# Performance work log

Measured on AMD Instinct MI355X. Metric: run time of the kernel, lower is better.

The kernel has to match this reference:

```python
import jax, jax.numpy as jnp
import numpy as np

N_NODES = 10000
N_EDGES = 100000
C = 64          # in_channels == out_channels (required by x_i + x_m)
D_EDGE = 16     # edge_attr feature dim


def setup_inputs() -> dict:
    key = jax.random.key(0)
    k_x, k_ei, k_ea, k_w, k_b, k_r, k_bias = jax.random.split(key, 7)
    x = jax.random.normal(k_x, (N_NODES, C), dtype=jnp.float32)
    edge_index = jax.random.randint(k_ei, (2, N_EDGES), 0, N_NODES, dtype=jnp.int32)
    edge_attr = jax.random.normal(k_ea, (N_EDGES, D_EDGE), dtype=jnp.float32)
    # nn = Linear(D_EDGE -> C*C), producing per-edge [C, C] weight matrices
    W_nn = jax.random.normal(k_w, (D_EDGE, C * C), dtype=jnp.float32) * (1.0 / np.sqrt(D_EDGE))
    b_nn = jax.random.normal(k_b, (C * C,), dtype=jnp.float32) * 0.01
    root = jax.random.normal(k_r, (C, C), dtype=jnp.float32) * (1.0 / np.sqrt(C))
    bias = jax.random.normal(k_bias, (C,), dtype=jnp.float32) * 0.01
    return {"x": x, "edge_index": edge_index, "edge_attr": edge_attr,
            "W_nn": W_nn, "b_nn": b_nn, "root": root, "bias": bias}


def reference(x, edge_index, edge_attr, W_nn, b_nn, root, bias):
    N, Cc = x.shape
    row, col = edge_index[0], edge_index[1]
    # per-edge weight matrices from nn(edge_attr): [E, C, C]
    e = (edge_attr @ W_nn + b_nn).reshape(-1, Cc, Cc)
    # gather source features and apply edge-conditioned matmul: [E, C]
    m = jnp.einsum('ec,eco->eo', x[row], e)
    # Faithful to torch loop: x_m[i] = m[col == i].mean() -> SCALAR mean over
    # all elements of incoming messages, broadcast across the feature row.
    seg_sum = jax.ops.segment_sum(m.sum(axis=1), col, num_segments=N)       # [N]
    cnt = jax.ops.segment_sum(jnp.ones_like(col, dtype=x.dtype), col,
                              num_segments=N) * Cc                            # [N]
    mean = jnp.where(cnt > 0, seg_sum / jnp.maximum(cnt, 1.0), 0.0)          # [N]
    x_m = jnp.broadcast_to(mean[:, None], (N, Cc))                            # [N, C]
    # root transform + bias
    out = x @ root + bias + x_m
    return out
```

## Files before the change

### kernel.cpp

```cpp
#include <hip/hip_runtime.h>
#include <hip/hip_bf16.h>


#define CC 64
#define DE 16
#define PAD 65

__global__ __launch_bounds__(128) void k_node_v(const float* __restrict__ W,
                                                const float* __restrict__ b,
                                                const float* __restrict__ x,
                                                float* __restrict__ v,
                                                float* __restrict__ bx,
                                                int N) {
    __shared__ float ws[1024 + CC];
    const int tid = threadIdx.x;

    for (int p = tid; p < 1024 + CC; p += 128) {
        const float4* src = (p < 1024) ? (const float4*)(W + (size_t)p * CC)
                                       : (const float4*)(b + (size_t)(p - 1024) * CC);
        float s = 0.f;
#pragma unroll
        for (int i = 0; i < 16; ++i) { float4 t = src[i]; s += t.x + t.y + t.z + t.w; }
        ws[p] = s;
    }
    __syncthreads();

    int n = blockIdx.x * 128 + tid;
    if (n >= N) return;

    const float4* x4 = (const float4*)(x + (size_t)n * CC);
    float4 xv[16];
#pragma unroll
    for (int i = 0; i < 16; ++i) xv[i] = x4[i];

    const float4* ws4 = (const float4*)ws;
    const float4* bs4 = (const float4*)(ws + 1024);

    float bs = 0.f;
#pragma unroll
    for (int c4 = 0; c4 < 16; ++c4) {
        float4 w = bs4[c4];
        bs += w.x * xv[c4].x + w.y * xv[c4].y + w.z * xv[c4].z + w.w * xv[c4].w;
    }
    bx[n] = bs;

    float vd[DE];
#pragma unroll
    for (int d = 0; d < DE; ++d) {
        float s = 0.f;
#pragma unroll
        for (int c4 = 0; c4 < 16; ++c4) {
            float4 w = ws4[d * 16 + c4];
            s += w.x * xv[c4].x + w.y * xv[c4].y + w.z * xv[c4].z + w.w * xv[c4].w;
        }
        vd[d] = s;
    }
    float4* vo = (float4*)(v + (size_t)n * DE);
#pragma unroll
    for (int i = 0; i < 4; ++i)
        vo[i] = make_float4(vd[4 * i], vd[4 * i + 1], vd[4 * i + 2], vd[4 * i + 3]);
}

__global__ __launch_bounds__(256) void k_edge(const int* __restrict__ ei,
                                              const float* __restrict__ ea,
                                              const float* __restrict__ v,
                                              const float* __restrict__ bx,
                                              float* __restrict__ seg,
                                              float* __restrict__ cnt,
                                              int E) {
    int e = blockIdx.x * 256 + threadIdx.x;
    if (e >= E) return;

    const int r  = ei[e];
    const int cn = ei[E + e];

    const float4* a4 = (const float4*)(ea + (size_t)e * DE);
    const float4* v4 = (const float4*)(v + (size_t)r * DE);

    float s = bx[r];
#pragma unroll
    for (int i = 0; i < 4; ++i) {
        float4 a = a4[i];
        float4 w = v4[i];
        s += a.x * w.x + a.y * w.y + a.z * w.z + a.w * w.w;
    }

    atomicAdd(seg + cn, s);
    atomicAdd(cnt + cn, 1.0f);
}

__global__ __launch_bounds__(256) void k_final(const float* __restrict__ x,
                                               const float* __restrict__ root,
                                               const float* __restrict__ bias,
                                               const float* __restrict__ seg,
                                               const float* __restrict__ cnt,
                                               float* __restrict__ out,
                                               int N) {
    __shared__ float rt[CC * CC];
    __shared__ float xs[16 * PAD];
    __shared__ float bi[CC];
    __shared__ float mn[16];
    int tid = threadIdx.x;
    int n0 = blockIdx.x * 16;

#pragma unroll
    for (int i = 0; i < 16; ++i) rt[tid + i * 256] = root[tid + i * 256];
#pragma unroll
    for (int it = 0; it < 4; ++it) {
        int i = it * 256 + tid;
        if ((size_t)n0 * CC + i < (size_t)N * CC)
            xs[(i >> 6) * PAD + (i & 63)] = x[(size_t)n0 * CC + i];
    }
    if (tid < CC) bi[tid] = bias[tid];
    if (tid < 16 && n0 + tid < N) {
        float c = cnt[n0 + tid];
        mn[tid] = c > 0.f ? seg[n0 + tid] / (c * (float)CC) : 0.f;
    }
    __syncthreads();

    int nl = tid >> 4, ci = tid & 15;
    int n = n0 + nl;
    if (n >= N) return;

    const float4* rt4 = (const float4*)rt;
    const float4* bi4 = (const float4*)bi;
    float m = mn[nl];
    float4 bv = bi4[ci];
    float4 acc = make_float4(bv.x + m, bv.y + m, bv.z + m, bv.w + m);
#pragma unroll
    for (int k = 0; k < CC; ++k) {
        float a  = xs[nl * PAD + k];
        float4 w = rt4[k * 16 + ci];
        acc.x += a * w.x; acc.y += a * w.y; acc.z += a * w.z; acc.w += a * w.w;
    }
    *(float4*)(out + (size_t)n * CC + ci * 4) = acc;
}

extern "C" void kernel_launch(void* const* d_in, const int* in_sizes, int n_in,
                              void* d_out, int out_size, void* d_ws, size_t ws_size,
                              hipStream_t stream) {
    const float* x    = (const float*)d_in[0];
    const int*   ei   = (const int*)  d_in[1];
    const float* ea   = (const float*)d_in[2];
    const float* W    = (const float*)d_in[3];
    const float* b    = (const float*)d_in[4];
    const float* root = (const float*)d_in[5];
    const float* bias = (const float*)d_in[6];
    float* out = (float*)d_out;
    float* ws  = (float*)d_ws;

    const int N = in_sizes[0] / CC;
    const int E = in_sizes[1] / 2;

    float* seg = ws;
    float* cnt = ws + N;
    float* v   = ws + 2 * N;
    float* bx  = ws + 2 * N + (size_t)N * DE;

    int vBlocks = (N + 127) / 128;
    int eBlocks = (E + 255) / 256;
    int fBlocks = (N + 15) / 16;

    k_node_v<<<vBlocks, 128, 0, stream>>>(W, b, x, v, bx, N);
    k_edge  <<<eBlocks, 256, 0, stream>>>(ei, ea, v, bx, seg, cnt, E);
    k_final <<<fBlocks, 256, 0, stream>>>(x, root, bias, seg, cnt, out, N);
}
```

Before: 106.7 us.

## Fuse node, edge and final stages into one persistent kernel with flag barriers

Merges the three launches (node projection, edge scatter, final root transform) into a single kernel. The first blocks compute the per-node projections and publish release flags. Every block computes its root matmul before waiting on those flags, then scatters its share of edges. A second all-block flag barrier guards the mean and the output write. This removes launch gaps and overlaps the root matmul with the producer stage. In exchange it relies on all 625 blocks being co-resident, since the spin barriers could deadlock otherwise. It also assumes the flag words start cleared on every call.

```diff
diff --git a/kernel.cpp b/kernel.cpp
--- a/kernel.cpp
+++ b/kernel.cpp
@@ -5,104 +5,75 @@
 #define CC 64
 #define DE 16
 #define PAD 65
+#define SENT 0x5CA1AB1Eu
 
-__global__ __launch_bounds__(128) void k_node_v(const float* __restrict__ W,
-                                                const float* __restrict__ b,
-                                                const float* __restrict__ x,
-                                                float* __restrict__ v,
-                                                float* __restrict__ bx,
-                                                int N) {
+__global__ __launch_bounds__(256, 3) void k_mega(
+    const float* __restrict__ W, const float* __restrict__ b,
+    const float* __restrict__ x, const int* __restrict__ ei,
+    const float* __restrict__ ea, const float* __restrict__ root,
+    const float* __restrict__ bias, float* __restrict__ out,
+    float* __restrict__ seg, float* __restrict__ cnt,
+    float* __restrict__ v, float* __restrict__ bx,
+    unsigned* __restrict__ flag1, unsigned* __restrict__ flag2,
+    int N, int E, int PROD, int EPB)
+{
     __shared__ float ws[1024 + CC];
-    const int tid = threadIdx.x;
-
-    for (int p = tid; p < 1024 + CC; p += 128) {
-        const float4* src = (p < 1024) ? (const float4*)(W + (size_t)p * CC)
-                                       : (const float4*)(b + (size_t)(p - 1024) * CC);
-        float s = 0.f;
-#pragma unroll
-        for (int i = 0; i < 16; ++i) { float4 t = src[i]; s += t.x + t.y + t.z + t.w; }
-        ws[p] = s;
-    }
-    __syncthreads();
-
-    int n = blockIdx.x * 128 + tid;
-    if (n >= N) return;
-
-    const float4* x4 = (const float4*)(x + (size_t)n * CC);
-    float4 xv[16];
-#pragma unroll
-    for (int i = 0; i < 16; ++i) xv[i] = x4[i];
-
-    const float4* ws4 = (const float4*)ws;
-    const float4* bs4 = (const float4*)(ws + 1024);
-
-    float bs = 0.f;
-#pragma unroll
-    for (int c4 = 0; c4 < 16; ++c4) {
-        float4 w = bs4[c4];
-        bs += w.x * xv[c4].x + w.y * xv[c4].y + w.z * xv[c4].z + w.w * xv[c4].w;
-    }
-    bx[n] = bs;
-
-    float vd[DE];
-#pragma unroll
-    for (int d = 0; d < DE; ++d) {
-        float s = 0.f;
-#pragma unroll
-        for (int c4 = 0; c4 < 16; ++c4) {
-            float4 w = ws4[d * 16 + c4];
-            s += w.x * xv[c4].x + w.y * xv[c4].y + w.z * xv[c4].z + w.w * xv[c4].w;
-        }
-        vd[d] = s;
-    }
-    float4* vo = (float4*)(v + (size_t)n * DE);
-#pragma unroll
-    for (int i = 0; i < 4; ++i)
-        vo[i] = make_float4(vd[4 * i], vd[4 * i + 1], vd[4 * i + 2], vd[4 * i + 3]);
-}
-
-__global__ __launch_bounds__(256) void k_edge(const int* __restrict__ ei,
-                                              const float* __restrict__ ea,
-                                              const float* __restrict__ v,
-                                              const float* __restrict__ bx,
-                                              float* __restrict__ seg,
-                                              float* __restrict__ cnt,
-                                              int E) {
-    int e = blockIdx.x * 256 + threadIdx.x;
-    if (e >= E) return;
-
-    const int r  = ei[e];
-    const int cn = ei[E + e];
-
-    const float4* a4 = (const float4*)(ea + (size_t)e * DE);
-    const float4* v4 = (const float4*)(v + (size_t)r * DE);
-
-    float s = bx[r];
-#pragma unroll
-    for (int i = 0; i < 4; ++i) {
-        float4 a = a4[i];
-        float4 w = v4[i];
-        s += a.x * w.x + a.y * w.y + a.z * w.z + a.w * w.w;
-    }
-
-    atomicAdd(seg + cn, s);
-    atomicAdd(cnt + cn, 1.0f);
-}
-
-__global__ __launch_bounds__(256) void k_final(const float* __restrict__ x,
-                                               const float* __restrict__ root,
-                                               const float* __restrict__ bias,
-                                               const float* __restrict__ seg,
-                                               const float* __restrict__ cnt,
-                                               float* __restrict__ out,
-                                               int N) {
     __shared__ float rt[CC * CC];
     __shared__ float xs[16 * PAD];
     __shared__ float bi[CC];
     __shared__ float mn[16];
-    int tid = threadIdx.x;
-    int n0 = blockIdx.x * 16;
+    const int tid = threadIdx.x;
+    const int bid = blockIdx.x;
+    const int nb  = gridDim.x;
 
+    if (bid < PROD) {
+        for (int p = tid; p < 1024 + CC; p += 256) {
+            const float4* src = (p < 1024) ? (const float4*)(W + (size_t)p * CC)
+                                           : (const float4*)(b + (size_t)(p - 1024) * CC);
+            float s = 0.f;
+#pragma unroll
+            for (int i = 0; i < 16; ++i) { float4 t = src[i]; s += t.x + t.y + t.z + t.w; }
+            ws[p] = s;
+        }
+        __syncthreads();
+        int n = bid * 256 + tid;
+        if (n < N) {
+            const float4* x4 = (const float4*)(x + (size_t)n * CC);
+            float4 xv[16];
+#pragma unroll
+            for (int i = 0; i < 16; ++i) xv[i] = x4[i];
+            const float4* ws4 = (const float4*)ws;
+            const float4* bs4 = (const float4*)(ws + 1024);
+            float bs = 0.f;
+#pragma unroll
+            for (int c4 = 0; c4 < 16; ++c4) {
+                float4 w = bs4[c4];
+                bs += w.x*xv[c4].x + w.y*xv[c4].y + w.z*xv[c4].z + w.w*xv[c4].w;
+            }
+            bx[n] = bs;
+            float vd[DE];
+#pragma unroll
+            for (int d = 0; d < DE; ++d) {
+                float s = 0.f;
+#pragma unroll
+                for (int c4 = 0; c4 < 16; ++c4) {
+                    float4 w = ws4[d * 16 + c4];
+                    s += w.x*xv[c4].x + w.y*xv[c4].y + w.z*xv[c4].z + w.w*xv[c4].w;
+                }
+                vd[d] = s;
+            }
+            float4* vo = (float4*)(v + (size_t)n * DE);
+#pragma unroll
+            for (int i = 0; i < 4; ++i)
+                vo[i] = make_float4(vd[4*i], vd[4*i+1], vd[4*i+2], vd[4*i+3]);
+        }
+        __syncthreads();
+        if (tid == 0)
+            __hip_atomic_store(&flag1[bid], SENT, __ATOMIC_RELEASE,
+                               __HIP_MEMORY_SCOPE_AGENT);
+    }
+
+    int n0 = bid * 16;
 #pragma unroll
     for (int i = 0; i < 16; ++i) rt[tid + i * 256] = root[tid + i * 256];
 #pragma unroll
@@ -112,28 +83,72 @@
             xs[(i >> 6) * PAD + (i & 63)] = x[(size_t)n0 * CC + i];
     }
     if (tid < CC) bi[tid] = bias[tid];
+    __syncthreads();
+    const int nl = tid >> 4, ci = tid & 15;
+    const int n = n0 + nl;
+    float4 acc = make_float4(0.f, 0.f, 0.f, 0.f);
+    if (n < N) {
+        const float4* rt4 = (const float4*)rt;
+        float4 bv = ((const float4*)bi)[ci];
+        acc = bv;
+#pragma unroll
+        for (int k = 0; k < CC; ++k) {
+            float a  = xs[nl * PAD + k];
+            float4 w = rt4[k * 16 + ci];
+            acc.x += a*w.x; acc.y += a*w.y; acc.z += a*w.z; acc.w += a*w.w;
+        }
+    }
+
+    if (tid < PROD) {
+        while (__hip_atomic_load(&flag1[tid], __ATOMIC_ACQUIRE,
+                                 __HIP_MEMORY_SCOPE_AGENT) != SENT)
+            __builtin_amdgcn_s_sleep(2);
+    }
+    __syncthreads();
+    if (tid == 0) __threadfence();
+    __syncthreads();
+
+    {
+        int e = bid * EPB + tid;
+        if (tid < EPB && e < E) {
+            const int r  = ei[e];
+            const int cn = ei[E + e];
+            const float4* a4 = (const float4*)(ea + (size_t)e * DE);
+            const float4* v4 = (const float4*)(v + (size_t)r * DE);
+            float s = bx[r];
+#pragma unroll
+            for (int i = 0; i < 4; ++i) {
+                float4 a = a4[i], wv = v4[i];
+                s += a.x*wv.x + a.y*wv.y + a.z*wv.z + a.w*wv.w;
+            }
+            atomicAdd(seg + cn, s);
+            atomicAdd(cnt + cn, 1.0f);
+        }
+    }
+
+    __syncthreads();
+    if (tid == 0)
+        __hip_atomic_store(&flag2[bid], SENT, __ATOMIC_RELEASE,
+                           __HIP_MEMORY_SCOPE_AGENT);
+    for (int f = tid; f < nb; f += 256) {
+        while (__hip_atomic_load(&flag2[f], __ATOMIC_ACQUIRE,
+                                 __HIP_MEMORY_SCOPE_AGENT) != SENT)
+            __builtin_amdgcn_s_sleep(2);
+    }
+    __syncthreads();
+    if (tid == 0) __threadfence();
+    __syncthreads();
+
     if (tid < 16 && n0 + tid < N) {
         float c = cnt[n0 + tid];
         mn[tid] = c > 0.f ? seg[n0 + tid] / (c * (float)CC) : 0.f;
     }
     __syncthreads();
-
-    int nl = tid >> 4, ci = tid & 15;
-    int n = n0 + nl;
-    if (n >= N) return;
-
-    const float4* rt4 = (const float4*)rt;
-    const float4* bi4 = (const float4*)bi;
-    float m = mn[nl];
-    float4 bv = bi4[ci];
-    float4 acc = make_float4(bv.x + m, bv.y + m, bv.z + m, bv.w + m);
-#pragma unroll
-    for (int k = 0; k < CC; ++k) {
-        float a  = xs[nl * PAD + k];
-        float4 w = rt4[k * 16 + ci];
-        acc.x += a * w.x; acc.y += a * w.y; acc.z += a * w.z; acc.w += a * w.w;
+    if (n < N) {
+        float m = mn[nl];
+        acc.x += m; acc.y += m; acc.z += m; acc.w += m;
+        *(float4*)(out + (size_t)n * CC + ci * 4) = acc;
     }
-    *(float4*)(out + (size_t)n * CC + ci * 4) = acc;
 }
 
 extern "C" void kernel_launch(void* const* d_in, const int* in_sizes, int n_in,
@@ -152,16 +167,18 @@
     const int N = in_sizes[0] / CC;
     const int E = in_sizes[1] / 2;
 
-    float* seg = ws;
-    float* cnt = ws + N;
-    float* v   = ws + 2 * N;
-    float* bx  = ws + 2 * N + (size_t)N * DE;
+    float*    seg   = ws;
+    float*    cnt   = ws + N;
+    float*    v     = ws + 2 * N;
+    float*    bx    = ws + 2 * N + (size_t)N * DE;
+    unsigned* flag1 = (unsigned*)(ws + 19 * (size_t)N);
+    unsigned* flag2 = flag1 + 64;
 
-    int vBlocks = (N + 127) / 128;
-    int eBlocks = (E + 255) / 256;
-    int fBlocks = (N + 15) / 16;
+    const int nb   = (N + 15) / 16;
+    const int PROD = (N + 255) / 256;
+    const int EPB  = (E + nb - 1) / nb;
 
-    k_node_v<<<vBlocks, 128, 0, stream>>>(W, b, x, v, bx, N);
-    k_edge  <<<eBlocks, 256, 0, stream>>>(ei, ea, v, bx, seg, cnt, E);
-    k_final <<<fBlocks, 256, 0, stream>>>(x, root, bias, seg, cnt, out, N);
+    k_mega<<<nb, 256, 0, stream>>>(W, b, x, ei, ea, root, bias, out,
+                                   seg, cnt, v, bx, flag1, flag2,
+                                   N, E, PROD, EPB);
 }
```

Result: slower. 298.2 us (+179.6%).
